# Optimization experiments

Measured on AMD Instinct MI355X. Metric: run time of the kernel, lower is better.

Reference implementation:

```python
import jax, jax.numpy as jnp
import numpy as np

N_HEADS = 16
ROPE_DIMS = 16
SEQ_LEN = 512


def _rope_cache(T, dtype=jnp.float32):
    rd = ROPE_DIMS
    freqs = 1.0 / (10000.0 ** (jnp.arange(0, rd, 2, dtype=jnp.float32) / rd))  # [rd/2]
    t = jnp.arange(T, dtype=jnp.float32)
    ang = jnp.outer(t, freqs)  # [T, rd/2]
    return jnp.cos(ang).astype(dtype), jnp.sin(ang).astype(dtype)


def _apply_rope(x, cos, sin):
    # x: [B, H, T, hd]; partial RoPE on first ROPE_DIMS dims
    rd = ROPE_DIMS
    x_rope, x_pass = x[..., :rd], x[..., rd:]
    x1, x2 = x_rope[..., : rd // 2], x_rope[..., rd // 2 :]
    # cos/sin: [T, rd/2] -> broadcast over B, H
    out = jnp.concatenate([x1 * cos - x2 * sin, x2 * cos + x1 * sin], axis=-1)
    return jnp.concatenate([out, x_pass], axis=-1)


def setup_inputs() -> dict:
    key = jax.random.key(0)
    k1, k2, k3 = jax.random.split(key, 3)
    B, T, C = 8, SEQ_LEN, 2048
    x = jax.random.normal(k1, (B, T, C), dtype=jnp.float32)
    Wqkv = jax.random.normal(k2, (3 * C, C), dtype=jnp.float32) * (1.0 / np.sqrt(C))
    Wout = jax.random.normal(k3, (C, C), dtype=jnp.float32) * (1.0 / np.sqrt(C))
    return {"x": x, "Wqkv": Wqkv, "Wout": Wout}


def reference(x, Wqkv, Wout):
    B, T, C = x.shape
    H = N_HEADS
    hd = C // H
    # fused QKV projection
    qkv = jnp.einsum("btc,fc->btf", x, Wqkv)  # [B, T, 3C]
    qkv = qkv.reshape(B, T, 3, H, hd)
    q, k, v = qkv[:, :, 0], qkv[:, :, 1], qkv[:, :, 2]  # [B, T, H, hd]
    q = jnp.transpose(q, (0, 2, 1, 3))  # [B, H, T, hd]
    k = jnp.transpose(k, (0, 2, 1, 3))
    v = jnp.transpose(v, (0, 2, 1, 3))
    cos, sin = _rope_cache(T, dtype=x.dtype)
    q = _apply_rope(q, cos, sin)
    k = _apply_rope(k, cos, sin)
    # causal SDPA
    scale = 1.0 / np.sqrt(hd)
    scores = jnp.einsum("bhqd,bhkd->bhqk", q, k) * scale
    causal = jnp.tril(jnp.ones((T, T), dtype=bool))
    scores = jnp.where(causal, scores, jnp.finfo(scores.dtype).min)
    attn = jax.nn.softmax(scores, axis=-1)
    y = jnp.einsum("bhqk,bhkd->bhqd", attn, v)  # [B, H, T, hd]
    y = jnp.transpose(y, (0, 2, 1, 3)).reshape(B, T, C)
    return jnp.einsum("btc,oc->bto", y, Wout)
```

## Files before the change

### kernel.cpp

```cpp
#include <hip/hip_runtime.h>

typedef __bf16 bf16_t;
typedef __bf16 bf16x4 __attribute__((ext_vector_type(4)));
typedef __bf16 bf16x8 __attribute__((ext_vector_type(8)));
typedef float f32x4 __attribute__((ext_vector_type(4)));

#define GLB(p) ((const __attribute__((address_space(1))) void*)(p))
#define LDS(p) ((__attribute__((address_space(3))) void*)(p))

__global__ void f32_to_bf16(const float* __restrict__ src, bf16_t* __restrict__ dst, int n8)
{
    const int i = blockIdx.x * 256 + threadIdx.x;
    if (i >= n8) return;
    const f32x4 a = *(const f32x4*)&src[(size_t)i * 8];
    const f32x4 b = *(const f32x4*)&src[(size_t)i * 8 + 4];
    bf16x8 h = {(bf16_t)a[0], (bf16_t)a[1], (bf16_t)a[2], (bf16_t)a[3],
                (bf16_t)b[0], (bf16_t)b[1], (bf16_t)b[2], (bf16_t)b[3]};
    *(bf16x8*)&dst[(size_t)i * 8] = h;
}

template <int MODE>
__global__ __launch_bounds__(256)
void gemm_bt(const bf16_t* __restrict__ A, const bf16_t* __restrict__ Bm, int K,
             bf16_t* __restrict__ o0, bf16_t* __restrict__ o1, bf16_t* __restrict__ o2,
             float* __restrict__ of)
{
    __shared__ __align__(16) bf16_t As[128 * 32];
    __shared__ __align__(16) bf16_t Bs[128 * 32];
    const int tid  = threadIdx.x;
    const int lane = tid & 63;
    const int w    = tid >> 6;
    const int wm   = (w & 1) * 64;
    const int wn   = (w >> 1) * 64;
    const int m0   = blockIdx.x * 128;
    const int n0   = blockIdx.y * 128;
    const int quad = lane >> 4;
    const int qcol = lane & 15;

    f32x4 acc[4][4];
#pragma unroll
    for (int i = 0; i < 4; ++i)
#pragma unroll
        for (int j = 0; j < 4; ++j)
            acc[i][j] = (f32x4){0.f, 0.f, 0.f, 0.f};

    const int rc = lane >> 2;
    const int cg = (lane & 3) ^ (rc & 3);
    const int c0 = 2 * w, c1 = 2 * w + 1;
    const bf16_t* ag0 = A  + (size_t)(m0 + 16 * c0 + rc) * K + cg * 8;
    const bf16_t* ag1 = A  + (size_t)(m0 + 16 * c1 + rc) * K + cg * 8;
    const bf16_t* bg0 = Bm + (size_t)(n0 + 16 * c0 + rc) * K + cg * 8;
    const bf16_t* bg1 = Bm + (size_t)(n0 + 16 * c1 + rc) * K + cg * 8;
    bf16_t* al0 = &As[c0 * 512];
    bf16_t* al1 = &As[c1 * 512];
    bf16_t* bl0 = &Bs[c0 * 512];
    bf16_t* bl1 = &Bs[c1 * 512];

    const int swz8 = (quad ^ (qcol & 3)) * 8;

    for (int k0 = 0; k0 < K; k0 += 32) {
        __syncthreads();
        __builtin_amdgcn_global_load_lds(GLB(ag0 + k0), LDS(al0), 16, 0, 0);
        __builtin_amdgcn_global_load_lds(GLB(ag1 + k0), LDS(al1), 16, 0, 0);
        __builtin_amdgcn_global_load_lds(GLB(bg0 + k0), LDS(bl0), 16, 0, 0);
        __builtin_amdgcn_global_load_lds(GLB(bg1 + k0), LDS(bl1), 16, 0, 0);
        __syncthreads();

        bf16x8 af[4], bf[4];
#pragma unroll
        for (int mt = 0; mt < 4; ++mt)
            af[mt] = *(const bf16x8*)&As[(wm + mt * 16 + qcol) * 32 + swz8];
#pragma unroll
        for (int nt = 0; nt < 4; ++nt)
            bf[nt] = *(const bf16x8*)&Bs[(wn + nt * 16 + qcol) * 32 + swz8];
#pragma unroll
        for (int mt = 0; mt < 4; ++mt)
#pragma unroll
            for (int nt = 0; nt < 4; ++nt)
                acc[mt][nt] = __builtin_amdgcn_mfma_f32_16x16x32_bf16(af[mt], bf[nt], acc[mt][nt], 0, 0, 0);
    }

#pragma unroll
    for (int mt = 0; mt < 4; ++mt) {
#pragma unroll
        for (int nt = 0; nt < 4; ++nt) {
#pragma unroll
            for (int r = 0; r < 4; ++r) {
                const int m = m0 + wm + mt * 16 + quad * 4 + r;
                const int f = n0 + wn + nt * 16 + qcol;
                const float val = acc[mt][nt][r];
                if (MODE == 0) {
                    const int b     = m >> 9;
                    const int t     = m & 511;
                    const int which = f >> 11;
                    const int h     = (f >> 7) & 15;
                    const int d     = f & 127;
                    if (which == 2) {
                        o2[((size_t)(((b << 4) + h) * 128 + d) << 9) + t] = (bf16_t)val;
                    } else {
                        bf16_t* dst = (which == 0) ? o0 : o1;
                        dst[(size_t)(((b << 4) + h) * 512 + t) * 128 + d] = (bf16_t)val;
                    }
                } else {
                    of[(size_t)m * 2048 + f] = val;
                }
            }
        }
    }
}

__global__ void rope_kernel(bf16_t* __restrict__ q, bf16_t* __restrict__ k)
{
    const int id  = blockIdx.x * 256 + threadIdx.x;
    const int arr = id >> 19;
    const int rem = id & ((1 << 19) - 1);
    const int bh  = rem >> 12;
    const int t   = (rem >> 3) & 511;
    const int d   = rem & 7;

    bf16_t* p = (arr ? k : q) + (size_t)(bh * 512 + t) * 128;
    const float x1 = (float)p[d];
    const float x2 = (float)p[d + 8];
    const float freq = __expf(-(float)d * 1.1512925464970229f);
    const float ang  = (float)t * freq;
    const float c = cosf(ang), s = sinf(ang);
    p[d]     = (bf16_t)(x1 * c - x2 * s);
    p[d + 8] = (bf16_t)(x2 * c + x1 * s);
}

#define KLD 136
#define VLD 72
#define PLD 72

__global__ __launch_bounds__(256)
void flash_attn(const bf16_t* __restrict__ q, const bf16_t* __restrict__ k,
                const bf16_t* __restrict__ vT, bf16_t* __restrict__ y)
{
    const int qtb = blockIdx.x;
    const int h   = blockIdx.y;
    const int b   = blockIdx.z;
    const int tid  = threadIdx.x;
    const int lane = tid & 63;
    const int w    = tid >> 6;
    const int quad = lane >> 4;
    const int qcol = lane & 15;

    __shared__ __align__(16) bf16_t Ks[64 * KLD];
    __shared__ __align__(16) bf16_t VTs[128 * VLD];
    __shared__ __align__(16) bf16_t Ps[128 * PLD];
    __shared__ __align__(16) float aS[4][2][16];
    __shared__ __align__(16) float lS[4][2][16];

    const bf16_t* qb  = q  + (size_t)((b * 16 + h) * 512) * 128;
    const bf16_t* kb  = k  + (size_t)((b * 16 + h) * 512) * 128;
    const bf16_t* vtb = vT + (size_t)((b * 16 + h) * 128) * 512;

    bf16x8 qfrag[2][4];
#pragma unroll
    for (int qg = 0; qg < 2; ++qg) {
        const int qrow = qtb * 128 + w * 32 + qg * 16 + qcol;
#pragma unroll
        for (int kc = 0; kc < 4; ++kc)
            qfrag[qg][kc] = *(const bf16x8*)&qb[(size_t)qrow * 128 + kc * 32 + quad * 8];
    }

    f32x4 acc_o[2][8];
#pragma unroll
    for (int qg = 0; qg < 2; ++qg)
#pragma unroll
        for (int nt = 0; nt < 8; ++nt) acc_o[qg][nt] = (f32x4){0.f, 0.f, 0.f, 0.f};
    float m_run[2] = {-INFINITY, -INFINITY};
    float l_run[2] = {0.f, 0.f};
    const float scale = 0.08838834764831845f;

    const int kt_last = 2 * qtb + 1;
    for (int kt = 0; kt <= kt_last; ++kt) {
        __syncthreads();
#pragma unroll
        for (int p = 0; p < 4; ++p) {
            const int r = p * 16 + (tid >> 4), c = (tid & 15) * 8;
            *(uint4*)&Ks[r * KLD + c] = *(const uint4*)&kb[(size_t)(kt * 64 + r) * 128 + c];
        }
#pragma unroll
        for (int p = 0; p < 4; ++p) {
            const int r = p * 32 + (tid >> 3), c = (tid & 7) * 8;
            *(uint4*)&VTs[r * VLD + c] = *(const uint4*)&vtb[(size_t)r * 512 + kt * 64 + c];
        }
        __syncthreads();

        const bool need_mask = (kt >= 2 * qtb);

#pragma unroll
        for (int qg = 0; qg < 2; ++qg) {
            f32x4 sacc[4];
#pragma unroll
            for (int mt = 0; mt < 4; ++mt) sacc[mt] = (f32x4){0.f, 0.f, 0.f, 0.f};
#pragma unroll
            for (int mt = 0; mt < 4; ++mt)
#pragma unroll
                for (int kc = 0; kc < 4; ++kc) {
                    bf16x8 af = *(const bf16x8*)&Ks[(mt * 16 + qcol) * KLD + kc * 32 + quad * 8];
                    sacc[mt] = __builtin_amdgcn_mfma_f32_16x16x32_bf16(af, qfrag[qg][kc], sacc[mt], 0, 0, 0);
                }

            float s[16];
#pragma unroll
            for (int mt = 0; mt < 4; ++mt)
#pragma unroll
                for (int r = 0; r < 4; ++r)
                    s[mt * 4 + r] = sacc[mt][r] * scale;
            if (need_mask) {
                const int qglob = qtb * 128 + w * 32 + qg * 16 + qcol;
#pragma unroll
                for (int mt = 0; mt < 4; ++mt)
#pragma unroll
                    for (int r = 0; r < 4; ++r)
                        if (kt * 64 + mt * 16 + quad * 4 + r > qglob)
                            s[mt * 4 + r] = -1e30f;
            }

            float mx = s[0];
#pragma unroll
            for (int i = 1; i < 16; ++i) mx = fmaxf(mx, s[i]);
            mx = fmaxf(mx, __shfl_xor(mx, 16));
            mx = fmaxf(mx, __shfl_xor(mx, 32));
            const float m_new = fmaxf(m_run[qg], mx);
            const float alpha = __expf(m_run[qg] - m_new);
            float p16[16];
            float sum = 0.f;
#pragma unroll
            for (int i = 0; i < 16; ++i) { p16[i] = __expf(s[i] - m_new); sum += p16[i]; }
            sum += __shfl_xor(sum, 16);
            sum += __shfl_xor(sum, 32);
            l_run[qg] = l_run[qg] * alpha + sum;
            m_run[qg] = m_new;
            if (quad == 0) aS[w][qg][qcol] = alpha;

#pragma unroll
            for (int mt = 0; mt < 4; ++mt) {
                bf16x4 pb = {(bf16_t)p16[mt * 4 + 0], (bf16_t)p16[mt * 4 + 1],
                             (bf16_t)p16[mt * 4 + 2], (bf16_t)p16[mt * 4 + 3]};
                *(bf16x4*)&Ps[(w * 32 + qg * 16 + qcol) * PLD + mt * 16 + quad * 4] = pb;
            }

            f32x4 alpha4 = *(const f32x4*)&aS[w][qg][quad * 4];
#pragma unroll
            for (int nt = 0; nt < 8; ++nt)
#pragma unroll
                for (int r = 0; r < 4; ++r)
                    acc_o[qg][nt][r] *= alpha4[r];

#pragma unroll
            for (int kc2 = 0; kc2 < 2; ++kc2) {
                bf16x8 pf = *(const bf16x8*)&Ps[(w * 32 + qg * 16 + qcol) * PLD + kc2 * 32 + quad * 8];
#pragma unroll
                for (int nt = 0; nt < 8; ++nt) {
                    bf16x8 vf = *(const bf16x8*)&VTs[(nt * 16 + qcol) * VLD + kc2 * 32 + quad * 8];
                    acc_o[qg][nt] = __builtin_amdgcn_mfma_f32_16x16x32_bf16(pf, vf, acc_o[qg][nt], 0, 0, 0);
                }
            }
        }
    }

    if (quad == 0) { lS[w][0][qcol] = l_run[0]; lS[w][1][qcol] = l_run[1]; }
#pragma unroll
    for (int qg = 0; qg < 2; ++qg) {
        f32x4 l4 = *(const f32x4*)&lS[w][qg][quad * 4];
#pragma unroll
        for (int nt = 0; nt < 8; ++nt)
#pragma unroll
            for (int r = 0; r < 4; ++r) {
                const int t  = qtb * 128 + w * 32 + qg * 16 + quad * 4 + r;
                const int cc = h * 128 + nt * 16 + qcol;
                y[(size_t)(b * 512 + t) * 2048 + cc] = (bf16_t)(acc_o[qg][nt][r] / l4[r]);
            }
    }
}

extern "C" void kernel_launch(void* const* d_in, const int* in_sizes, int n_in,
                              void* d_out, int out_size, void* d_ws, size_t ws_size,
                              hipStream_t stream)
{
    (void)in_sizes; (void)n_in; (void)out_size; (void)ws_size;

    const float* x    = (const float*)d_in[0];
    const float* Wqkv = (const float*)d_in[1];
    const float* Wout = (const float*)d_in[2];
    float* out = (float*)d_out;

    const size_t SEG = (size_t)8 * 16 * 512 * 128;
    bf16_t* q      = (bf16_t*)d_ws;
    bf16_t* k      = q + SEG;
    bf16_t* vT     = k + SEG;
    bf16_t* xb     = vT + SEG;
    bf16_t* y      = xb;
    bf16_t* Wqkvb  = xb + SEG;
    bf16_t* Woutb  = Wqkvb + (size_t)6144 * 2048;

    f32_to_bf16<<<(8388608 / 8) / 256, 256, 0, stream>>>(x, xb, 8388608 / 8);
    f32_to_bf16<<<(12582912 / 8) / 256, 256, 0, stream>>>(Wqkv, Wqkvb, 12582912 / 8);
    f32_to_bf16<<<(4194304 / 8) / 256, 256, 0, stream>>>(Wout, Woutb, 4194304 / 8);
    gemm_bt<0><<<dim3(4096 / 128, 6144 / 128), 256, 0, stream>>>(xb, Wqkvb, 2048, q, k, vT, nullptr);
    rope_kernel<<<(2 * 128 * 512 * 8) / 256, 256, 0, stream>>>(q, k);
    flash_attn<<<dim3(4, 16, 8), 256, 0, stream>>>(q, k, vT, y);
    gemm_bt<1><<<dim3(4096 / 128, 2048 / 128), 256, 0, stream>>>(y, Woutb, 2048, nullptr, nullptr, nullptr, out);
}
```

Measured before the change: 376.8 us.

## Replace 128x128 GEMM with double-buffered 256x256 tile, 8-wave pipelined kernel

```diff
diff --git a/kernel.cpp b/kernel.cpp
--- a/kernel.cpp
+++ b/kernel.cpp
@@ -19,75 +19,137 @@
     *(bf16x8*)&dst[(size_t)i * 8] = h;
 }
 
+#define LDB4(d, kk)                                                            \
+    { _Pragma("unroll") for (int nt = 0; nt < 4; ++nt)                         \
+        bfr[nt] = *(const bf16x8*)(sBb + (d) * 65536 + (kk) * 16384 + nt * 1024); }
+
+#define LDA4(d, kk, g)                                                         \
+    { _Pragma("unroll") for (int i = 0; i < 4; ++i)                            \
+        afr[i] = *(const bf16x8*)(sAb + (d) * 65536 + (kk) * 16384 + ((g) * 4 + i) * 1024); }
+
+#define MM4(g)                                                                 \
+    { _Pragma("unroll") for (int i = 0; i < 4; ++i)                            \
+        _Pragma("unroll") for (int nt = 0; nt < 4; ++nt)                       \
+            acc[(g) * 4 + i][nt] = __builtin_amdgcn_mfma_f32_16x16x32_bf16(    \
+                afr[i], bfr[nt], acc[(g) * 4 + i][nt], 0, 0, 0); }
+
+#define PHASE_TAIL(g)                                                          \
+    __builtin_amdgcn_s_barrier();                                              \
+    asm volatile("s_waitcnt lgkmcnt(0)" ::: "memory");                         \
+    __builtin_amdgcn_s_setprio(1);                                             \
+    MM4(g);                                                                    \
+    __builtin_amdgcn_s_setprio(0);                                             \
+    __builtin_amdgcn_s_barrier();
+
 template <int MODE>
-__global__ __launch_bounds__(256)
-void gemm_bt(const bf16_t* __restrict__ A, const bf16_t* __restrict__ Bm, int K,
+__global__ __launch_bounds__(512, 2)
+void gemm256(const bf16_t* __restrict__ A, const bf16_t* __restrict__ Bm, int K,
              bf16_t* __restrict__ o0, bf16_t* __restrict__ o1, bf16_t* __restrict__ o2,
              float* __restrict__ of)
 {
-    __shared__ __align__(16) bf16_t As[128 * 32];
-    __shared__ __align__(16) bf16_t Bs[128 * 32];
+    __shared__ __align__(16) bf16_t smem[65536];
+    char* smbase = (char*)smem;
+
     const int tid  = threadIdx.x;
     const int lane = tid & 63;
     const int w    = tid >> 6;
-    const int wm   = (w & 1) * 64;
-    const int wn   = (w >> 1) * 64;
-    const int m0   = blockIdx.x * 128;
-    const int n0   = blockIdx.y * 128;
+    const int wr   = w >> 2;
+    const int wc   = w & 3;
     const int quad = lane >> 4;
     const int qcol = lane & 15;
-
-    f32x4 acc[4][4];
-#pragma unroll
-    for (int i = 0; i < 4; ++i)
+    const int m0   = blockIdx.x * 256;
+    const int n0   = blockIdx.y * 256;
+
+    f32x4 acc[8][4];
+#pragma unroll
+    for (int i = 0; i < 8; ++i)
 #pragma unroll
         for (int j = 0; j < 4; ++j)
             acc[i][j] = (f32x4){0.f, 0.f, 0.f, 0.f};
 
-    const int rc = lane >> 2;
-    const int cg = (lane & 3) ^ (rc & 3);
-    const int c0 = 2 * w, c1 = 2 * w + 1;
-    const bf16_t* ag0 = A  + (size_t)(m0 + 16 * c0 + rc) * K + cg * 8;
-    const bf16_t* ag1 = A  + (size_t)(m0 + 16 * c1 + rc) * K + cg * 8;
-    const bf16_t* bg0 = Bm + (size_t)(n0 + 16 * c0 + rc) * K + cg * 8;
-    const bf16_t* bg1 = Bm + (size_t)(n0 + 16 * c1 + rc) * K + cg * 8;
-    bf16_t* al0 = &As[c0 * 512];
-    bf16_t* al1 = &As[c1 * 512];
-    bf16_t* bl0 = &Bs[c0 * 512];
-    bf16_t* bl1 = &Bs[c1 * 512];
-
-    const int swz8 = (quad ^ (qcol & 3)) * 8;
-
-    for (int k0 = 0; k0 < K; k0 += 32) {
-        __syncthreads();
-        __builtin_amdgcn_global_load_lds(GLB(ag0 + k0), LDS(al0), 16, 0, 0);
-        __builtin_amdgcn_global_load_lds(GLB(ag1 + k0), LDS(al1), 16, 0, 0);
-        __builtin_amdgcn_global_load_lds(GLB(bg0 + k0), LDS(bl0), 16, 0, 0);
-        __builtin_amdgcn_global_load_lds(GLB(bg1 + k0), LDS(bl1), 16, 0, 0);
-        __syncthreads();
-
-        bf16x8 af[4], bf[4];
-#pragma unroll
-        for (int mt = 0; mt < 4; ++mt)
-            af[mt] = *(const bf16x8*)&As[(wm + mt * 16 + qcol) * 32 + swz8];
-#pragma unroll
-        for (int nt = 0; nt < 4; ++nt)
-            bf[nt] = *(const bf16x8*)&Bs[(wn + nt * 16 + qcol) * 32 + swz8];
-#pragma unroll
-        for (int mt = 0; mt < 4; ++mt)
-#pragma unroll
-            for (int nt = 0; nt < 4; ++nt)
-                acc[mt][nt] = __builtin_amdgcn_mfma_f32_16x16x32_bf16(af[mt], bf[nt], acc[mt][nt], 0, 0, 0);
-    }
-
-#pragma unroll
-    for (int mt = 0; mt < 4; ++mt) {
+    const int srow = w * 16 + (lane >> 2);
+    const int scg  = (lane & 3) ^ ((lane >> 2) & 3);
+    const bf16_t* Ag = A  + (size_t)(m0 + srow) * K + scg * 8;
+    const bf16_t* Bg = Bm + (size_t)(n0 + srow) * K + scg * 8;
+
+    auto STAGE = [&](int d, int t, int hh) {
+        const int isA = hh & 1;
+        const int kh  = hh >> 1;
+        const bf16_t* g = (isA ? Ag : Bg) + t * 64 + kh * 32;
+        char* l = smbase + d * 65536 + kh * 16384 + (isA ? 0 : 32768) + w * 1024;
+        __builtin_amdgcn_global_load_lds(GLB(g), LDS(l), 16, 0, 0);
+        __builtin_amdgcn_global_load_lds(GLB(g + (size_t)128 * K), LDS(l + 8192), 16, 0, 0);
+    };
+
+    const int rswz = (quad ^ (qcol & 3)) << 4;
+    const char* sAb = smbase + (wr * 128 + qcol) * 64 + rswz;
+    const char* sBb = smbase + 32768 + (wc * 64 + qcol) * 64 + rswz;
+
+    bf16x8 afr[4], bfr[4];
+
+    const int NT  = K >> 6;
+    const int NIT = NT >> 1;
+
+    STAGE(0, 0, 0); STAGE(0, 0, 1); STAGE(0, 0, 2); STAGE(0, 0, 3);
+    STAGE(1, 1, 0); STAGE(1, 1, 1); STAGE(1, 1, 2);
+    asm volatile("s_waitcnt vmcnt(6)" ::: "memory");
+    __builtin_amdgcn_s_barrier();
+
+    for (int J = 0; J < NIT - 1; ++J) {
+        const int t = 2 * J;
+        LDB4(0, 0); LDA4(0, 0, 0); STAGE(1, t + 1, 3);
+        PHASE_TAIL(0);
+        LDA4(0, 0, 1); STAGE(0, t + 2, 0);
+        PHASE_TAIL(1);
+        LDB4(0, 1); LDA4(0, 1, 0); STAGE(0, t + 2, 1);
+        PHASE_TAIL(0);
+        LDA4(0, 1, 1); STAGE(0, t + 2, 2);
+        asm volatile("s_waitcnt vmcnt(6)" ::: "memory");
+        PHASE_TAIL(1);
+        LDB4(1, 0); LDA4(1, 0, 0); STAGE(0, t + 2, 3);
+        PHASE_TAIL(0);
+        LDA4(1, 0, 1); STAGE(1, t + 3, 0);
+        PHASE_TAIL(1);
+        LDB4(1, 1); LDA4(1, 1, 0); STAGE(1, t + 3, 1);
+        PHASE_TAIL(0);
+        LDA4(1, 1, 1); STAGE(1, t + 3, 2);
+        asm volatile("s_waitcnt vmcnt(6)" ::: "memory");
+        PHASE_TAIL(1);
+    }
+
+    {
+        const int t = NT - 2;
+        LDB4(0, 0); LDA4(0, 0, 0); STAGE(1, t + 1, 3);
+        PHASE_TAIL(0);
+        LDA4(0, 0, 1);
+        PHASE_TAIL(1);
+        LDB4(0, 1); LDA4(0, 1, 0);
+        PHASE_TAIL(0);
+        LDA4(0, 1, 1);
+        asm volatile("s_waitcnt vmcnt(0)" ::: "memory");
+        PHASE_TAIL(1);
+        LDB4(1, 0); LDA4(1, 0, 0);
+        PHASE_TAIL(0);
+        LDA4(1, 0, 1);
+        PHASE_TAIL(1);
+        LDB4(1, 1); LDA4(1, 1, 0);
+        PHASE_TAIL(0);
+        LDA4(1, 1, 1);
+        __builtin_amdgcn_s_barrier();
+        asm volatile("s_waitcnt lgkmcnt(0)" ::: "memory");
+        __builtin_amdgcn_s_setprio(1);
+        MM4(1);
+        __builtin_amdgcn_s_setprio(0);
+    }
+
+#pragma unroll
+    for (int mt = 0; mt < 8; ++mt) {
 #pragma unroll
         for (int nt = 0; nt < 4; ++nt) {
 #pragma unroll
             for (int r = 0; r < 4; ++r) {
-                const int m = m0 + wm + mt * 16 + quad * 4 + r;
-                const int f = n0 + wn + nt * 16 + qcol;
+                const int m = m0 + wr * 128 + mt * 16 + quad * 4 + r;
+                const int f = n0 + wc * 64 + nt * 16 + qcol;
                 const float val = acc[mt][nt][r];
                 if (MODE == 0) {
                     const int b     = m >> 9;
@@ -300,8 +362,8 @@
     f32_to_bf16<<<(8388608 / 8) / 256, 256, 0, stream>>>(x, xb, 8388608 / 8);
     f32_to_bf16<<<(12582912 / 8) / 256, 256, 0, stream>>>(Wqkv, Wqkvb, 12582912 / 8);
     f32_to_bf16<<<(4194304 / 8) / 256, 256, 0, stream>>>(Wout, Woutb, 4194304 / 8);
-    gemm_bt<0><<<dim3(4096 / 128, 6144 / 128), 256, 0, stream>>>(xb, Wqkvb, 2048, q, k, vT, nullptr);
+    gemm256<0><<<dim3(4096 / 256, 6144 / 256), 512, 0, stream>>>(xb, Wqkvb, 2048, q, k, vT, nullptr);
     rope_kernel<<<(2 * 128 * 512 * 8) / 256, 256, 0, stream>>>(q, k);
     flash_attn<<<dim3(4, 16, 8), 256, 0, stream>>>(q, k, vT, y);
-    gemm_bt<1><<<dim3(4096 / 128, 2048 / 128), 256, 0, stream>>>(y, Woutb, 2048, nullptr, nullptr, nullptr, out);
-}
+    gemm256<1><<<dim3(4096 / 256, 2048 / 256), 512, 0, stream>>>(y, Woutb, 2048, nullptr, nullptr, nullptr, out);
+}
```

New measurement: 377.0 us. No clear change (+0.0%).
